# Performance work log

Measured on AMD Instinct MI355X. Metric: run time of the kernel, lower is better.

The kernel has to match this reference:

```python
import jax, jax.numpy as jnp
import numpy as np

N, C, H, W = 8, 256, 128, 128
K = 7            # cls_p
HID = 10         # hidden_dim
OUT_C = (K - 1) * HID  # 60
BN_EPS = 1e-5


def setup_inputs() -> dict:
    key = jax.random.key(0)
    ks = jax.random.split(key, 7)
    return {
        "p_fea": jax.random.normal(ks[0], (N, C, H, W), jnp.float32),
        "p_seg": jax.random.normal(ks[1], (N, K, H, W), jnp.float32),
        "Wq": jax.random.normal(ks[2], (HID, C), jnp.float32) * 0.05,
        "bq": jax.random.normal(ks[3], (HID,), jnp.float32) * 0.05,
        "Wk": jax.random.normal(ks[4], (HID, C), jnp.float32) * 0.05,
        "bk": jax.random.normal(ks[5], (HID,), jnp.float32) * 0.05,
        "Wp": jax.random.normal(ks[6], (OUT_C, 2 * C), jnp.float32) * 0.05,
        "gamma": jnp.ones((OUT_C,), jnp.float32),
        "beta": jnp.zeros((OUT_C,), jnp.float32),
    }


def reference(p_fea, p_seg, Wq, bq, Wk, bk, Wp, gamma, beta):
    n, c, h, w = p_fea.shape
    hw = h * w
    fea = p_fea.reshape(n, c, hw)                      # [n,c,s]
    # class-center pooling: softmax over class dim, weighted mean of features
    att = jax.nn.softmax(p_seg.reshape(n, K, hw), axis=1)      # [n,k,s]
    num = jnp.einsum('ncs,nks->nck', fea, att)                 # [n,c,k]
    den = jnp.sum(att, axis=2)[:, None, :]                     # [n,1,k]
    p_center = num / den                                        # [n,c,k]
    # 1x1 conv1d / conv2d == matmul over channel dim
    query = jnp.einsum('oc,nck->nok', Wq, p_center) + bq[None, :, None]  # [n,hid,k]
    key_ = jnp.einsum('oc,ncs->nos', Wk, fea) + bk[None, :, None]        # [n,hid,s]
    energy = jnp.einsum('nok,nos->nks', query, key_)                     # [n,k,s]
    attention = jax.nn.softmax(energy, axis=1)                           # over class dim
    new_fea = jnp.einsum('nck,nks->ncs', p_center, attention).reshape(n, c, h, w)
    # project: concat -> 1x1 conv (no bias) -> BN (batch stats) -> ReLU
    x = jnp.concatenate([p_fea, new_fea], axis=1)              # [n,2c,h,w]
    y = jnp.einsum('oc,nchw->nohw', Wp, x)                     # [n,60,h,w]
    mean = jnp.mean(y, axis=(0, 2, 3))
    var = jnp.var(y, axis=(0, 2, 3))
    y = (y - mean[None, :, None, None]) * jax.lax.rsqrt(var + BN_EPS)[None, :, None, None]
    y = y * gamma[None, :, None, None] + beta[None, :, None, None]
    y = jnp.maximum(y, 0.0)
    # torch.split(..., HID, dim=1) -> list of (cls_p-1) chunks; return as one axis
    return y.reshape(n, K - 1, HID, h, w)
```

## Files before the change

kernel.cpp:

```cpp
#include <hip/hip_runtime.h>
#include <hip/hip_bf16.h>

#define N_    8
#define C_    256
#define K_    7
#define HID_  10
#define OUTC_ 60
#define S_    16384
#define BN_EPS 1e-5f

#define OFF_PP     0
#define OFF_DP     1048576
#define OFF_EB     1052672
#define OFF_WB16   1052736
#define OFF_M2B    1151040
#define OFF_PART   1153600
#define OFF_SCL    1276480
#define OFF_SHF    1276544
#define OFF_Y16    1276608

#define GLDS(g, l) __builtin_amdgcn_global_load_lds( \
    (const __attribute__((address_space(1))) unsigned int*)(g), \
    (__attribute__((address_space(3))) unsigned int*)(l), 16, 0, 0)

typedef __attribute__((ext_vector_type(8))) short bfrag;
typedef __attribute__((ext_vector_type(4))) float f32x4;

static __device__ __forceinline__ unsigned short f2bf(float f) {
    __hip_bfloat16 h = __float2bfloat16(f);
    return *reinterpret_cast<unsigned short*>(&h);
}
static __device__ __forceinline__ float bfh2f(unsigned int u) {
    return __builtin_bit_cast(float, u & 0xffff0000u);
}
static __device__ __forceinline__ float bfl2f(unsigned int u) {
    return __builtin_bit_cast(float, u << 16);
}

__global__ void __launch_bounds__(256) k_pool(
        const float* __restrict__ fea, const float* __restrict__ seg,
        float* __restrict__ pp, float* __restrict__ dp) {
    int g = blockIdx.x;
    int lin = (g & 7) * 64 + (g >> 3);
    int n = lin >> 6, sl = lin & 63;
    int tid = threadIdx.x, lane = tid & 63, wv = tid >> 6;
    int r15 = lane & 15, kg = (lane >> 4) << 3, pg = (lane >> 4) << 2;
    int px0 = sl * 256;

    __shared__ unsigned short attT[16 * 256];
    __shared__ unsigned short feaB[2][256 * 32];
    __shared__ float red[4][8];

    {
        const float* sp = seg + (size_t)n * K_ * S_ + px0 + tid;
        float e[K_], mx = -1e30f;
#pragma unroll
        for (int k = 0; k < K_; k++) { e[k] = sp[(size_t)k * S_]; mx = fmaxf(mx, e[k]); }
        float sum = 0.f;
#pragma unroll
        for (int k = 0; k < K_; k++) { e[k] = __expf(e[k] - mx); sum += e[k]; }
        float inv = 1.f / sum;
#pragma unroll
        for (int k = 0; k < K_; k++) {
            e[k] *= inv;
            attT[k * 256 + tid] = f2bf(e[k]);
        }
#pragma unroll
        for (int k = 0; k < K_; k++) {
            float v = e[k];
            for (int off = 32; off; off >>= 1) v += __shfl_xor(v, off, 64);
            if (lane == 0) red[wv][k] = v;
        }
    }

    const float* fb = fea + (size_t)n * C_ * S_ + px0;
    int pq4 = (tid & 7) * 4;
    int crow = tid >> 3;

    {
        float4 s[8];
#pragma unroll
        for (int rr = 0; rr < 8; rr++)
            s[rr] = *(const float4*)(fb + (size_t)(rr * 32 + crow) * S_ + pq4);
#pragma unroll
        for (int rr = 0; rr < 8; rr++) {
            unsigned int u0 = (unsigned int)f2bf(s[rr].x) | ((unsigned int)f2bf(s[rr].y) << 16);
            unsigned int u1 = (unsigned int)f2bf(s[rr].z) | ((unsigned int)f2bf(s[rr].w) << 16);
            *(uint2*)&feaB[0][(rr * 32 + crow) * 32 + pq4] = make_uint2(u0, u1);
        }
    }
    __syncthreads();
    if (tid < K_)
        dp[(size_t)lin * 8 + tid] = red[0][tid] + red[1][tid] + red[2][tid] + red[3][tid];

    f32x4 acc[4];
#pragma unroll
    for (int mt = 0; mt < 4; mt++) acc[mt] = (f32x4)0.f;

#pragma unroll
    for (int ch = 0; ch < 8; ch++) {
        int cur = ch & 1;
        float4 s[8];
        if (ch < 7) {
#pragma unroll
            for (int rr = 0; rr < 8; rr++)
                s[rr] = *(const float4*)(fb + (size_t)(rr * 32 + crow) * S_ + (ch + 1) * 32 + pq4);
        }
        bfrag b = *(const bfrag*)&attT[r15 * 256 + ch * 32 + kg];
#pragma unroll
        for (int mt = 0; mt < 4; mt++) {
            bfrag a = *(const bfrag*)&feaB[cur][(wv * 64 + mt * 16 + r15) * 32 + kg];
            acc[mt] = __builtin_amdgcn_mfma_f32_16x16x32_bf16(a, b, acc[mt], 0, 0, 0);
        }
        if (ch < 7) {
#pragma unroll
            for (int rr = 0; rr < 8; rr++) {
                unsigned int u0 = (unsigned int)f2bf(s[rr].x) | ((unsigned int)f2bf(s[rr].y) << 16);
                unsigned int u1 = (unsigned int)f2bf(s[rr].z) | ((unsigned int)f2bf(s[rr].w) << 16);
                *(uint2*)&feaB[cur ^ 1][(rr * 32 + crow) * 32 + pq4] = make_uint2(u0, u1);
            }
        }
        __syncthreads();
    }

    if (r15 < K_) {
#pragma unroll
        for (int mt = 0; mt < 4; mt++) {
#pragma unroll
            for (int r = 0; r < 4; r++) {
                int c = wv * 64 + mt * 16 + pg + r;
                pp[((size_t)lin * 256 + c) * 8 + r15] = acc[mt][r];
            }
        }
    }
}

__global__ void k_center(const float* __restrict__ pp, const float* __restrict__ dp,
                         const float* __restrict__ Wq, const float* __restrict__ bq,
                         const float* __restrict__ Wk, const float* __restrict__ bk,
                         const float* __restrict__ Wp,
                         float* __restrict__ eb, float* __restrict__ m2b,
                         float* __restrict__ wb16) {
    int n = blockIdx.x >> 3, j = blockIdx.x & 7;
    int tid = threadIdx.x;
    __shared__ float pc[C_ * K_];
    __shared__ float ql[HID_ * K_];
    __shared__ float dinv[K_];
    if (tid < K_) {
        float d = 0.f;
        for (int s = 0; s < 64; s++) d += dp[(size_t)(n * 64 + s) * 8 + tid];
        dinv[tid] = 1.f / d;
    }
    __syncthreads();
    for (int i = tid; i < C_ * K_; i += 256) {
        int c = i / K_, k = i - c * K_;
        float v = 0.f;
        for (int s = 0; s < 64; s++)
            v += pp[((size_t)(n * 64 + s) * 256 + c) * 8 + k];
        pc[i] = v * dinv[k];
    }
    __syncthreads();
    if (tid < HID_ * K_) {
        int o = tid / K_, k = tid % K_;
        float s = bq[o];
        for (int c = 0; c < C_; c++) s += Wq[o * C_ + c] * pc[c * K_ + k];
        ql[tid] = s;
    }
    __syncthreads();
    unsigned short* wp16 = (unsigned short*)wb16 + (size_t)n * 24576;
    for (int i = j * 3072 + tid; i < (j + 1) * 3072; i += 256) {
        int ch = i / 6144, r = i - ch * 6144;
        int o = r / 72, jj = r - o * 72;
        float v = 0.f;
        if (o < 80 && jj < 64) {
            int c = ch * 64 + jj;
            if (o < 60) v = Wp[o * 2 * C_ + c];
            else if (o < 67) {
                int k = o - 60;
                for (int o2 = 0; o2 < HID_; o2++) v += ql[o2 * K_ + k] * Wk[o2 * C_ + c];
            }
        }
        wp16[i] = f2bf(v);
    }
    unsigned short* mp16 = (unsigned short*)m2b + (size_t)n * 640;
    if (tid < 80) {
        int i = j * 80 + tid;
        int o = i >> 3, k = i & 7;
        float v = 0.f;
        if (k < 7 && o < 60) {
            for (int c = 0; c < C_; c++) v += Wp[o * 2 * C_ + C_ + c] * pc[c * K_ + k];
        }
        mp16[i] = f2bf(v);
    }
    if (j == 0 && tid < K_) {
        float s = 0.f;
        for (int o = 0; o < HID_; o++) s += ql[o * K_ + tid] * bk[o];
        eb[n * K_ + tid] = s;
    }
}

__global__ void __launch_bounds__(256) k_main(
        const float* __restrict__ fea, const float* __restrict__ wb16,
        const float* __restrict__ ebias, const float* __restrict__ m2b,
        unsigned short* __restrict__ y16, float* __restrict__ part) {
    int g = blockIdx.x;
    int lin = (g & 7) * 128 + (g >> 3);
    int n = lin >> 7, tile = lin & 127;
    int tid = threadIdx.x, lane = tid & 63, wv = tid >> 6;
    int r15 = lane & 15, kg = (lane >> 4) << 3, pg = (lane >> 4) << 2;

    __shared__ unsigned short wlds[2][6144];
    __shared__ unsigned short feaT[2][9216];
    __shared__ unsigned short abf[128 * 8];
    __shared__ unsigned short m2l[640];
    __shared__ float att_e[K_][128];
    __shared__ float ebl[8];
    __shared__ float redm[4][80];
    __shared__ float redq[4][80];

    const unsigned int* wsrc = (const unsigned int*)wb16 + (size_t)n * 12288;
    const unsigned int* m2s  = (const unsigned int*)m2b + (size_t)n * 320;
    for (int i = tid; i < 320; i += 256) ((unsigned int*)m2l)[i] = m2s[i];
    if (tid < K_) ebl[tid] = ebias[n * K_ + tid];

    const float* fbase = fea + (size_t)n * C_ * S_ + tile * 128;
    int cr2 = tid >> 3, h = tid & 7;

    f32x4 acc[5][2];
#pragma unroll
    for (int ot = 0; ot < 5; ot++) { acc[ot][0] = (f32x4)0.f; acc[ot][1] = (f32x4)0.f; }

    auto ldw = [&](int ch, int buf) {
#pragma unroll
        for (int rnd = 0; rnd < 3; rnd++)
            GLDS(wsrc + ch * 3072 + rnd * 1024 + wv * 256 + lane * 4,
                 &((unsigned int*)wlds[buf])[rnd * 1024 + wv * 256]);
    };
    auto ldfea = [&](int ch, float4* s0, float4* s1) {
        const float* bp = fbase + (size_t)(ch * 64 + cr2 * 2) * S_ + h * 16;
#pragma unroll
        for (int i = 0; i < 4; i++) s0[i] = *(const float4*)(bp + i * 4);
#pragma unroll
        for (int i = 0; i < 4; i++) s1[i] = *(const float4*)(bp + S_ + i * 4);
    };
    auto wrfea = [&](int buf, const float4* s0, const float4* s1) {
        unsigned int* dst = (unsigned int*)feaT[buf];
#pragma unroll
        for (int i = 0; i < 4; i++)
#pragma unroll
            for (int e = 0; e < 4; e++) {
                int px = h * 16 + i * 4 + e;
                dst[px * 36 + cr2] = (unsigned int)f2bf(((const float*)&s0[i])[e])
                                   | ((unsigned int)f2bf(((const float*)&s1[i])[e]) << 16);
            }
    };
    auto mfma = [&](int buf) {
        const unsigned short* fb = feaT[buf];
        const unsigned short* wb = wlds[buf];
#pragma unroll
        for (int ks = 0; ks < 2; ks++) {
            bfrag a0 = *(const bfrag*)&fb[(wv * 32 + r15) * 72 + ks * 32 + kg];
            bfrag a1 = *(const bfrag*)&fb[(wv * 32 + 16 + r15) * 72 + ks * 32 + kg];
#pragma unroll
            for (int ot = 0; ot < 5; ot++) {
                bfrag b = *(const bfrag*)&wb[(ot * 16 + r15) * 72 + ks * 32 + kg];
                acc[ot][0] = __builtin_amdgcn_mfma_f32_16x16x32_bf16(a0, b, acc[ot][0], 0, 0, 0);
                acc[ot][1] = __builtin_amdgcn_mfma_f32_16x16x32_bf16(a1, b, acc[ot][1], 0, 0, 0);
            }
        }
    };
#define WAITBAR(nvm) asm volatile("s_waitcnt vmcnt(" #nvm ") lgkmcnt(0)" ::: "memory"); \
                     __builtin_amdgcn_s_barrier();

    float4 A0[4], A1[4], B0[4], B1[4];
    ldw(0, 0);
    ldfea(0, A0, A1);
    ldfea(1, B0, B1);
    wrfea(0, A0, A1);
    WAITBAR(8)

    wrfea(1, B0, B1);
    ldw(1, 1);
    ldfea(2, A0, A1);
    mfma(0);
    WAITBAR(8)

    wrfea(0, A0, A1);
    ldw(2, 0);
    ldfea(3, B0, B1);
    mfma(1);
    WAITBAR(8)

    wrfea(1, B0, B1);
    ldw(3, 1);
    mfma(0);
    WAITBAR(0)

    mfma(1);
#undef WAITBAR

    if (r15 >= 12) {
        int k = r15 - 12;
#pragma unroll
        for (int pxt = 0; pxt < 2; pxt++)
#pragma unroll
            for (int r = 0; r < 4; r++)
                att_e[k][wv * 32 + pxt * 16 + pg + r] = acc[3][pxt][r];
    }
    if (r15 < 3) {
        int k = 4 + r15;
#pragma unroll
        for (int pxt = 0; pxt < 2; pxt++)
#pragma unroll
            for (int r = 0; r < 4; r++)
                att_e[k][wv * 32 + pxt * 16 + pg + r] = acc[4][pxt][r];
    }
    __syncthreads();
    if (tid < 128) {
        float e[K_], mx = -1e30f;
#pragma unroll
        for (int k = 0; k < K_; k++) { e[k] = att_e[k][tid] + ebl[k]; mx = fmaxf(mx, e[k]); }
        float sum = 0.f;
#pragma unroll
        for (int k = 0; k < K_; k++) { e[k] = __expf(e[k] - mx); sum += e[k]; }
        float inv = 1.f / sum;
        unsigned int* ab = (unsigned int*)abf;
        ab[tid * 4 + 0] = (unsigned int)f2bf(e[0] * inv) | ((unsigned int)f2bf(e[1] * inv) << 16);
        ab[tid * 4 + 1] = (unsigned int)f2bf(e[2] * inv) | ((unsigned int)f2bf(e[3] * inv) << 16);
        ab[tid * 4 + 2] = (unsigned int)f2bf(e[4] * inv) | ((unsigned int)f2bf(e[5] * inv) << 16);
        ab[tid * 4 + 3] = (unsigned int)f2bf(e[6] * inv);
    }
    __syncthreads();

    bfrag az = (bfrag)(short)0;
    bfrag a20 = az, a21 = az;
    if (lane < 16) {
        a20 = *(const bfrag*)&abf[(wv * 32 + r15) * 8];
        a21 = *(const bfrag*)&abf[(wv * 32 + 16 + r15) * 8];
    }
#pragma unroll
    for (int ot = 0; ot < 5; ot++) {
        bfrag b2 = az;
        if (lane < 16) b2 = *(const bfrag*)&m2l[(ot * 16 + r15) * 8];
        acc[ot][0] = __builtin_amdgcn_mfma_f32_16x16x32_bf16(a20, b2, acc[ot][0], 0, 0, 0);
        acc[ot][1] = __builtin_amdgcn_mfma_f32_16x16x32_bf16(a21, b2, acc[ot][1], 0, 0, 0);
    }

    unsigned short* ybase = y16 + (size_t)n * OUTC_ * S_ + tile * 128 + wv * 32 + pg;
#pragma unroll
    for (int ot = 0; ot < 5; ot++) {
        int o = ot * 16 + r15;
        float sm_ = 0.f, sq_ = 0.f;
#pragma unroll
        for (int pxt = 0; pxt < 2; pxt++) {
            f32x4 v = acc[ot][pxt];
            if (o < OUTC_) {
                unsigned int u0 = (unsigned int)f2bf(v[0]) | ((unsigned int)f2bf(v[1]) << 16);
                unsigned int u1 = (unsigned int)f2bf(v[2]) | ((unsigned int)f2bf(v[3]) << 16);
                *(uint2*)(ybase + (size_t)o * S_ + pxt * 16) = make_uint2(u0, u1);
            }
            sm_ += v[0] + v[1] + v[2] + v[3];
            sq_ += v[0]*v[0] + v[1]*v[1] + v[2]*v[2] + v[3]*v[3];
        }
        sm_ += __shfl_xor(sm_, 16, 64); sm_ += __shfl_xor(sm_, 32, 64);
        sq_ += __shfl_xor(sq_, 16, 64); sq_ += __shfl_xor(sq_, 32, 64);
        if (lane < 16) { redm[wv][ot * 16 + lane] = sm_; redq[wv][ot * 16 + lane] = sq_; }
    }
    __syncthreads();
    if (tid < 120) {
        float s;
        if (tid < OUTC_)
            s = redm[0][tid] + redm[1][tid] + redm[2][tid] + redm[3][tid];
        else {
            int o = tid - OUTC_;
            s = redq[0][o] + redq[1][o] + redq[2][o] + redq[3][o];
        }
        part[(size_t)g * 120 + tid] = s;
    }
}

__global__ void k_bn(const float* __restrict__ part, const float* __restrict__ gamma,
                     const float* __restrict__ beta, float* __restrict__ scl,
                     float* __restrict__ shf) {
    int t = threadIdx.x & 127, q = threadIdx.x >> 7;
    __shared__ float red[4][120];
    __shared__ float tot[120];
    if (t < 120) {
        float s = 0.f;
        for (int b = q * 256; b < q * 256 + 256; b++) s += part[(size_t)b * 120 + t];
        red[q][t] = s;
    }
    __syncthreads();
    if (threadIdx.x < 120)
        tot[threadIdx.x] = red[0][threadIdx.x] + red[1][threadIdx.x] +
                           red[2][threadIdx.x] + red[3][threadIdx.x];
    __syncthreads();
    if (threadIdx.x < OUTC_) {
        const float invn = 1.f / (float)(N_ * S_);
        float mean = tot[threadIdx.x] * invn;
        float var = tot[60 + threadIdx.x] * invn - mean * mean;
        float sc = gamma[threadIdx.x] * rsqrtf(var + BN_EPS);
        scl[threadIdx.x] = sc;
        shf[threadIdx.x] = beta[threadIdx.x] - mean * sc;
    }
}

__global__ void k_apply(const unsigned short* __restrict__ y16,
                        const float* __restrict__ scl, const float* __restrict__ shf,
                        float* __restrict__ out) {
    int idx = blockIdx.x * 256 + threadIdx.x;
    int o = (idx >> 11) % OUTC_;
    uint4 v = ((const uint4*)y16)[idx];
    float a = scl[o], b = shf[o];
    float4 r0, r1;
    r0.x = fmaxf(bfl2f(v.x) * a + b, 0.f);
    r0.y = fmaxf(bfh2f(v.x) * a + b, 0.f);
    r0.z = fmaxf(bfl2f(v.y) * a + b, 0.f);
    r0.w = fmaxf(bfh2f(v.y) * a + b, 0.f);
    r1.x = fmaxf(bfl2f(v.z) * a + b, 0.f);
    r1.y = fmaxf(bfh2f(v.z) * a + b, 0.f);
    r1.z = fmaxf(bfl2f(v.w) * a + b, 0.f);
    r1.w = fmaxf(bfh2f(v.w) * a + b, 0.f);
    ((float4*)out)[idx * 2 + 0] = r0;
    ((float4*)out)[idx * 2 + 1] = r1;
}

extern "C" void kernel_launch(void* const* d_in, const int* in_sizes, int n_in,
                              void* d_out, int out_size, void* d_ws, size_t ws_size,
                              hipStream_t stream) {
    const float* p_fea = (const float*)d_in[0];
    const float* p_seg = (const float*)d_in[1];
    const float* Wq    = (const float*)d_in[2];
    const float* bq    = (const float*)d_in[3];
    const float* Wk    = (const float*)d_in[4];
    const float* bk    = (const float*)d_in[5];
    const float* Wp    = (const float*)d_in[6];
    const float* gamma = (const float*)d_in[7];
    const float* beta  = (const float*)d_in[8];

    float* ws   = (float*)d_ws;
    float* pp   = ws + OFF_PP;
    float* dp   = ws + OFF_DP;
    float* eb   = ws + OFF_EB;
    float* wb16 = ws + OFF_WB16;
    float* m2b  = ws + OFF_M2B;
    float* part = ws + OFF_PART;
    float* scl  = ws + OFF_SCL;
    float* shf  = ws + OFF_SHF;
    unsigned short* y16 = (unsigned short*)(ws + OFF_Y16);
    float* ybuf = (float*)d_out;

    k_pool<<<512, 256, 0, stream>>>(p_fea, p_seg, pp, dp);
    k_center<<<64, 256, 0, stream>>>(pp, dp, Wq, bq, Wk, bk, Wp, eb, m2b, wb16);
    k_main<<<1024, 256, 0, stream>>>(p_fea, wb16, eb, m2b, y16, part);
    k_bn<<<1, 512, 0, stream>>>(part, gamma, beta, scl, shf);
    k_apply<<<(N_ * OUTC_ * S_ / 8) / 256, 256, 0, stream>>>(y16, scl, shf, ybuf);
}
```

Measured before the change: 113.9 us.

## Split pooling over channel halves and fuse BN stats via atomics into apply

k_pool now launches 1024 blocks, each covering half the channels, and restructures its double-buffered prefetch to load two chunks ahead with a raw barrier. The separate single-block k_bn kernel is removed: k_main atomically accumulates the per-channel sums into a total buffer (zeroed in k_center), and k_apply computes scale and shift in shared memory per block. The goal is to raise occupancy in the pooling stage and remove one serial launch plus the reduction over 1024 partials. In exchange the softmax over the segmentation map is computed twice per pixel slice, and the float atomics make the summation order nondeterministic.

```diff
diff --git a/kernel.cpp b/kernel.cpp
--- a/kernel.cpp
+++ b/kernel.cpp
@@ -14,10 +14,8 @@
 #define OFF_EB     1052672
 #define OFF_WB16   1052736
 #define OFF_M2B    1151040
-#define OFF_PART   1153600
-#define OFF_SCL    1276480
-#define OFF_SHF    1276544
-#define OFF_Y16    1276608
+#define OFF_TOT    1153600
+#define OFF_Y16    1153728
 
 #define GLDS(g, l) __builtin_amdgcn_global_load_lds( \
     (const __attribute__((address_space(1))) unsigned int*)(g), \
@@ -41,14 +39,16 @@
         const float* __restrict__ fea, const float* __restrict__ seg,
         float* __restrict__ pp, float* __restrict__ dp) {
     int g = blockIdx.x;
-    int lin = (g & 7) * 64 + (g >> 3);
-    int n = lin >> 6, sl = lin & 63;
+    int lin = (g & 7) * 128 + (g >> 3);
+    int n = lin >> 7, r = lin & 127;
+    int sl = r >> 1, h2 = r & 1;
+    int c0 = h2 * 128;
+    int px0 = sl * 256;
     int tid = threadIdx.x, lane = tid & 63, wv = tid >> 6;
     int r15 = lane & 15, kg = (lane >> 4) << 3, pg = (lane >> 4) << 2;
-    int px0 = sl * 256;
 
     __shared__ unsigned short attT[16 * 256];
-    __shared__ unsigned short feaB[2][256 * 32];
+    __shared__ unsigned short feaB[2][128 * 32];
     __shared__ float red[4][8];
 
     {
@@ -73,63 +73,61 @@
         }
     }
 
-    const float* fb = fea + (size_t)n * C_ * S_ + px0;
+    const float* fb = fea + ((size_t)n * C_ + c0) * S_ + px0;
     int pq4 = (tid & 7) * 4;
     int crow = tid >> 3;
 
-    {
-        float4 s[8];
-#pragma unroll
-        for (int rr = 0; rr < 8; rr++)
-            s[rr] = *(const float4*)(fb + (size_t)(rr * 32 + crow) * S_ + pq4);
-#pragma unroll
-        for (int rr = 0; rr < 8; rr++) {
+    auto ldc = [&](int ch, float4* s) {
+#pragma unroll
+        for (int rr = 0; rr < 4; rr++)
+            s[rr] = *(const float4*)(fb + (size_t)(rr * 32 + crow) * S_ + ch * 32 + pq4);
+    };
+    auto wrc = [&](int buf, const float4* s) {
+#pragma unroll
+        for (int rr = 0; rr < 4; rr++) {
             unsigned int u0 = (unsigned int)f2bf(s[rr].x) | ((unsigned int)f2bf(s[rr].y) << 16);
             unsigned int u1 = (unsigned int)f2bf(s[rr].z) | ((unsigned int)f2bf(s[rr].w) << 16);
-            *(uint2*)&feaB[0][(rr * 32 + crow) * 32 + pq4] = make_uint2(u0, u1);
-        }
-    }
-    __syncthreads();
-    if (tid < K_)
-        dp[(size_t)lin * 8 + tid] = red[0][tid] + red[1][tid] + red[2][tid] + red[3][tid];
-
-    f32x4 acc[4];
-#pragma unroll
-    for (int mt = 0; mt < 4; mt++) acc[mt] = (f32x4)0.f;
+            *(uint2*)&feaB[buf][(rr * 32 + crow) * 32 + pq4] = make_uint2(u0, u1);
+        }
+    };
+
+    float4 A[4], B[4];
+    ldc(0, A);
+    wrc(0, A);
+    ldc(1, B);
+    __syncthreads();
+    if (h2 == 0 && tid < K_)
+        dp[(size_t)(n * 64 + sl) * 8 + tid] =
+            red[0][tid] + red[1][tid] + red[2][tid] + red[3][tid];
+
+    f32x4 acc[2];
+    acc[0] = (f32x4)0.f; acc[1] = (f32x4)0.f;
 
 #pragma unroll
     for (int ch = 0; ch < 8; ch++) {
-        int cur = ch & 1;
-        float4 s[8];
-        if (ch < 7) {
-#pragma unroll
-            for (int rr = 0; rr < 8; rr++)
-                s[rr] = *(const float4*)(fb + (size_t)(rr * 32 + crow) * S_ + (ch + 1) * 32 + pq4);
-        }
+        if (ch > 0) {
+            asm volatile("s_waitcnt lgkmcnt(0)" ::: "memory");
+            __builtin_amdgcn_s_barrier();
+        }
+        float4* issue = (ch & 1) ? B : A;
+        float4* wsrc2 = (ch & 1) ? A : B;
+        if (ch < 6) ldc(ch + 2, issue);
+        if (ch < 7) wrc((ch + 1) & 1, wsrc2);
         bfrag b = *(const bfrag*)&attT[r15 * 256 + ch * 32 + kg];
 #pragma unroll
-        for (int mt = 0; mt < 4; mt++) {
-            bfrag a = *(const bfrag*)&feaB[cur][(wv * 64 + mt * 16 + r15) * 32 + kg];
+        for (int mt = 0; mt < 2; mt++) {
+            bfrag a = *(const bfrag*)&feaB[ch & 1][(wv * 32 + mt * 16 + r15) * 32 + kg];
             acc[mt] = __builtin_amdgcn_mfma_f32_16x16x32_bf16(a, b, acc[mt], 0, 0, 0);
         }
-        if (ch < 7) {
-#pragma unroll
-            for (int rr = 0; rr < 8; rr++) {
-                unsigned int u0 = (unsigned int)f2bf(s[rr].x) | ((unsigned int)f2bf(s[rr].y) << 16);
-                unsigned int u1 = (unsigned int)f2bf(s[rr].z) | ((unsigned int)f2bf(s[rr].w) << 16);
-                *(uint2*)&feaB[cur ^ 1][(rr * 32 + crow) * 32 + pq4] = make_uint2(u0, u1);
-            }
-        }
-        __syncthreads();
-    }
-
-    if (r15 < K_) {
-#pragma unroll
-        for (int mt = 0; mt < 4; mt++) {
-#pragma unroll
-            for (int r = 0; r < 4; r++) {
-                int c = wv * 64 + mt * 16 + pg + r;
-                pp[((size_t)lin * 256 + c) * 8 + r15] = acc[mt][r];
+    }
+
+    if (r15 < 8) {
+#pragma unroll
+        for (int mt = 0; mt < 2; mt++) {
+#pragma unroll
+            for (int rr = 0; rr < 4; rr++) {
+                int c = c0 + wv * 32 + mt * 16 + pg + rr;
+                pp[((size_t)(n * 64 + sl) * 256 + c) * 8 + r15] = acc[mt][rr];
             }
         }
     }
@@ -140,9 +138,10 @@
                          const float* __restrict__ Wk, const float* __restrict__ bk,
                          const float* __restrict__ Wp,
                          float* __restrict__ eb, float* __restrict__ m2b,
-                         float* __restrict__ wb16) {
+                         float* __restrict__ wb16, float* __restrict__ tot) {
     int n = blockIdx.x >> 3, j = blockIdx.x & 7;
     int tid = threadIdx.x;
+    if (blockIdx.x == 0 && tid < 128) tot[tid] = 0.f;
     __shared__ float pc[C_ * K_];
     __shared__ float ql[HID_ * K_];
     __shared__ float dinv[K_];
@@ -202,7 +201,7 @@
 __global__ void __launch_bounds__(256) k_main(
         const float* __restrict__ fea, const float* __restrict__ wb16,
         const float* __restrict__ ebias, const float* __restrict__ m2b,
-        unsigned short* __restrict__ y16, float* __restrict__ part) {
+        unsigned short* __restrict__ y16, float* __restrict__ tot) {
     int g = blockIdx.x;
     int lin = (g & 7) * 128 + (g >> 3);
     int n = lin >> 7, tile = lin & 127;
@@ -375,43 +374,29 @@
             int o = tid - OUTC_;
             s = redq[0][o] + redq[1][o] + redq[2][o] + redq[3][o];
         }
-        part[(size_t)g * 120 + tid] = s;
-    }
-}
-
-__global__ void k_bn(const float* __restrict__ part, const float* __restrict__ gamma,
-                     const float* __restrict__ beta, float* __restrict__ scl,
-                     float* __restrict__ shf) {
-    int t = threadIdx.x & 127, q = threadIdx.x >> 7;
-    __shared__ float red[4][120];
-    __shared__ float tot[120];
-    if (t < 120) {
-        float s = 0.f;
-        for (int b = q * 256; b < q * 256 + 256; b++) s += part[(size_t)b * 120 + t];
-        red[q][t] = s;
-    }
-    __syncthreads();
-    if (threadIdx.x < 120)
-        tot[threadIdx.x] = red[0][threadIdx.x] + red[1][threadIdx.x] +
-                           red[2][threadIdx.x] + red[3][threadIdx.x];
-    __syncthreads();
-    if (threadIdx.x < OUTC_) {
+        atomicAdd(&tot[tid], s);
+    }
+}
+
+__global__ void k_apply(const unsigned short* __restrict__ y16,
+                        const float* __restrict__ tot,
+                        const float* __restrict__ gamma, const float* __restrict__ beta,
+                        float* __restrict__ out) {
+    __shared__ float sscl[OUTC_], sshf[OUTC_];
+    int tid = threadIdx.x;
+    if (tid < OUTC_) {
         const float invn = 1.f / (float)(N_ * S_);
-        float mean = tot[threadIdx.x] * invn;
-        float var = tot[60 + threadIdx.x] * invn - mean * mean;
-        float sc = gamma[threadIdx.x] * rsqrtf(var + BN_EPS);
-        scl[threadIdx.x] = sc;
-        shf[threadIdx.x] = beta[threadIdx.x] - mean * sc;
-    }
-}
-
-__global__ void k_apply(const unsigned short* __restrict__ y16,
-                        const float* __restrict__ scl, const float* __restrict__ shf,
-                        float* __restrict__ out) {
-    int idx = blockIdx.x * 256 + threadIdx.x;
+        float mean = tot[tid] * invn;
+        float var = tot[60 + tid] * invn - mean * mean;
+        float sc = gamma[tid] * rsqrtf(var + BN_EPS);
+        sscl[tid] = sc;
+        sshf[tid] = beta[tid] - mean * sc;
+    }
+    __syncthreads();
+    int idx = blockIdx.x * 256 + tid;
     int o = (idx >> 11) % OUTC_;
     uint4 v = ((const uint4*)y16)[idx];
-    float a = scl[o], b = shf[o];
+    float a = sscl[o], b = sshf[o];
     float4 r0, r1;
     r0.x = fmaxf(bfl2f(v.x) * a + b, 0.f);
     r0.y = fmaxf(bfh2f(v.x) * a + b, 0.f);
@@ -444,15 +429,12 @@
     float* eb   = ws + OFF_EB;
     float* wb16 = ws + OFF_WB16;
     float* m2b  = ws + OFF_M2B;
-    float* part = ws + OFF_PART;
-    float* scl  = ws + OFF_SCL;
-    float* shf  = ws + OFF_SHF;
+    float* tot  = ws + OFF_TOT;
     unsigned short* y16 = (unsigned short*)(ws + OFF_Y16);
     float* ybuf = (float*)d_out;
 
-    k_pool<<<512, 256, 0, stream>>>(p_fea, p_seg, pp, dp);
-    k_center<<<64, 256, 0, stream>>>(pp, dp, Wq, bq, Wk, bk, Wp, eb, m2b, wb16);
-    k_main<<<1024, 256, 0, stream>>>(p_fea, wb16, eb, m2b, y16, part);
-    k_bn<<<1, 512, 0, stream>>>(part, gamma, beta, scl, shf);
-    k_apply<<<(N_ * OUTC_ * S_ / 8) / 256, 256, 0, stream>>>(y16, scl, shf, ybuf);
-}
+    k_pool<<<1024, 256, 0, stream>>>(p_fea, p_seg, pp, dp);
+    k_center<<<64, 256, 0, stream>>>(pp, dp, Wq, bq, Wk, bk, Wp, eb, m2b, wb16, tot);
+    k_main<<<1024, 256, 0, stream>>>(p_fea, wb16, eb, m2b, y16, tot);
+    k_apply<<<(N_ * OUTC_ * S_ / 8) / 256, 256, 0, stream>>>(y16, tot, gamma, beta, ybuf);
+}
```

Result: slower. 118.3 us (+3.8%).
